# Optimization experiments

Hardware: AMD Instinct MI355X
Metric: run time of the kernel (lower is better)

Reference implementation:

```python
import jax, jax.numpy as jnp
import numpy as np

D_MODEL = 768
N_HEAD = 12


def setup_inputs() -> dict:
    key = jax.random.key(0)
    k1, k2, k3, k4, k5 = jax.random.split(key, 5)
    B, T, C = 4, 2048, D_MODEL
    s = 1.0 / np.sqrt(C)
    return {
        "x": jax.random.normal(k1, (B, T, C), dtype=jnp.float32),
        "w_attn": jax.random.normal(k2, (C, 3 * C), dtype=jnp.float32) * s,
        "b_attn": jax.random.normal(k3, (3 * C,), dtype=jnp.float32) * 0.02,
        "w_proj": jax.random.normal(k4, (C, C), dtype=jnp.float32) * s,
        "b_proj": jax.random.normal(k5, (C,), dtype=jnp.float32) * 0.02,
    }


def reference(x, w_attn, b_attn, w_proj, b_proj):
    B, T, C = x.shape
    H = N_HEAD
    Dh = C // H
    qkv = x @ w_attn + b_attn                      # [B, T, 3C]
    q, k, v = jnp.split(qkv, 3, axis=-1)
    # [B, H, T, Dh]
    q = q.reshape(B, T, H, Dh).transpose(0, 2, 1, 3)
    k = k.reshape(B, T, H, Dh).transpose(0, 2, 1, 3)
    v = v.reshape(B, T, H, Dh).transpose(0, 2, 1, 3)
    att = jnp.einsum("bhqd,bhkd->bhqk", q, k) * (1.0 / np.sqrt(Dh))
    causal = jnp.tril(jnp.ones((T, T), dtype=bool))
    att = jnp.where(causal[None, None, :, :], att, -jnp.inf)
    att = jax.nn.softmax(att, axis=-1)             # dropout p=0 (eval)
    y = jnp.einsum("bhqk,bhkd->bhqd", att, v)      # [B, H, T, Dh]
    y = y.transpose(0, 2, 1, 3).reshape(B, T, C)
    return y @ w_proj + b_proj
```

## Files before the change

kernel.cpp:

```cpp
#include <hip/hip_runtime.h>
#include <stdint.h>

#define NHEAD 12
#define DH 64
#define BATCH 4
#define SEQ 2048
#define CDIM 768
#define MROWS (BATCH*SEQ)

typedef __attribute__((ext_vector_type(8))) short short8;
typedef __attribute__((ext_vector_type(4))) float floatx4;
typedef unsigned int u32;

__device__ inline unsigned short f2bf(float f) {
    union { float f; unsigned u; } v; v.f = f;
    unsigned r = v.u + 0x7FFFu + ((v.u >> 16) & 1u);
    return (unsigned short)(r >> 16);
}

__device__ __forceinline__ u32 pk_bf16(float a, float b) {
    u32 d;
    asm("v_cvt_pk_bf16_f32 %0, %1, %2" : "=v"(d) : "v"(a), "v"(b));
    return d;
}

__device__ __forceinline__ void async_cp16(const unsigned short* g, unsigned short* l) {
    __builtin_amdgcn_global_load_lds(
        (const __attribute__((address_space(1))) u32*)g,
        (__attribute__((address_space(3))) u32*)l, 16, 0, 0);
}

__global__ void convert_f32_bf16(const float* __restrict__ in,
                                 unsigned short* __restrict__ out, int n) {
    int i = (blockIdx.x * blockDim.x + threadIdx.x) * 4;
    if (i + 3 < n) {
        float4 f = *(const float4*)(in + i);
        union { unsigned short s[4]; uint2 u; } p;
        p.s[0] = f2bf(f.x); p.s[1] = f2bf(f.y);
        p.s[2] = f2bf(f.z); p.s[3] = f2bf(f.w);
        *(uint2*)(out + i) = p.u;
    }
}

__global__ __launch_bounds__(256) void transpose_conv(
    const float* __restrict__ in, unsigned short* __restrict__ out,
    int K, int N) {
    __shared__ unsigned short T[64][72];
    const int k0 = blockIdx.x * 64, n0 = blockIdx.y * 64;
    const int t = threadIdx.x;
    const int nc = t & 63, kw = t >> 6;
    for (int i = 0; i < 16; i++) {
        const int kr = kw + i * 4;
        T[nc][kr] = f2bf(in[(size_t)(k0 + kr) * N + n0 + nc]);
    }
    __syncthreads();
    const int row = t >> 2, seg = t & 3;
    uint4 a = *(const uint4*)&T[row][seg * 16];
    uint4 b2 = *(const uint4*)&T[row][seg * 16 + 8];
    unsigned short* o = &out[(size_t)(n0 + row) * K + k0 + seg * 16];
    *(uint4*)o = a;
    *(uint4*)(o + 8) = b2;
}

template<int MODE>
__global__ __launch_bounds__(256) void gemm_bf16(
    const unsigned short* __restrict__ A,
    const unsigned short* __restrict__ BT,
    const float* __restrict__ bias,
    float* __restrict__ Cout,
    unsigned short* __restrict__ Qout,
    unsigned short* __restrict__ Kout,
    unsigned short* __restrict__ VTout,
    int Ndim, int Kdim)
{
    __shared__ unsigned short As[2][128 * 32];
    __shared__ unsigned short Bs[2][128 * 32];
    const int tid  = threadIdx.x;
    const int wave = tid >> 6;
    const int lane = tid & 63;
    const int l16  = lane & 15;
    const int quad = lane >> 4;
    const int wm = wave >> 1, wn = wave & 1;
    const int m0 = blockIdx.x * 128;
    const int n0 = blockIdx.y * 128;

    const int rloc = lane >> 2;
    const int gs   = ((lane & 3) ^ (rloc & 3) ^ ((rloc >> 2) & 3)) * 8;
    const int ar0  = wave * 32 + rloc;
    const int pg = ((quad ^ (l16 & 3) ^ ((l16 >> 2) & 3))) * 8;

    floatx4 acc[4][4];
    for (int i = 0; i < 4; i++)
        for (int j = 0; j < 4; j++) acc[i][j] = (floatx4)0.0f;

    for (int ch = 0; ch < 2; ch++) {
        const int row = ar0 + ch * 16;
        async_cp16(&A[(size_t)(m0 + row) * Kdim + gs], &As[0][(wave * 2 + ch) * 512]);
        async_cp16(&BT[(size_t)(n0 + row) * Kdim + gs], &Bs[0][(wave * 2 + ch) * 512]);
    }
    __syncthreads();

    for (int k0 = 0; k0 < Kdim; k0 += 32) {
        const int cur = (k0 >> 5) & 1;
        if (k0 + 32 < Kdim) {
            for (int ch = 0; ch < 2; ch++) {
                const int row = ar0 + ch * 16;
                async_cp16(&A[(size_t)(m0 + row) * Kdim + k0 + 32 + gs],
                           &As[cur ^ 1][(wave * 2 + ch) * 512]);
                async_cp16(&BT[(size_t)(n0 + row) * Kdim + k0 + 32 + gs],
                           &Bs[cur ^ 1][(wave * 2 + ch) * 512]);
            }
        }
        short8 a[4], b[4];
        for (int i = 0; i < 4; i++)
            a[i] = *(const short8*)&As[cur][(wm * 64 + i * 16 + l16) * 32 + pg];
        for (int j = 0; j < 4; j++)
            b[j] = *(const short8*)&Bs[cur][(wn * 64 + j * 16 + l16) * 32 + pg];
        for (int i = 0; i < 4; i++)
            for (int j = 0; j < 4; j++)
                acc[i][j] = __builtin_amdgcn_mfma_f32_16x16x32_bf16(
                    a[i], b[j], acc[i][j], 0, 0, 0);
        __syncthreads();
    }

    const float QSCALE = 0.18033688011112042f;
    for (int i = 0; i < 4; i++) {
        const int mbase = m0 + wm * 64 + i * 16 + quad * 4;
        for (int j = 0; j < 4; j++) {
            const int ncol = n0 + wn * 64 + j * 16 + l16;
            const float bv = bias[ncol];
            for (int r = 0; r < 4; r++) {
                const int m = mbase + r;
                const float v = acc[i][j][r] + bv;
                if (MODE == 0) {
                    Cout[(size_t)m * Ndim + ncol] = v;
                } else {
                    const int b_  = m >> 11, t = m & 2047;
                    const int part = ncol / CDIM;
                    const int c = ncol - part * CDIM;
                    const int h = c >> 6, d = c & 63;
                    const size_t bh = (size_t)(b_ * NHEAD + h);
                    if (part == 0)
                        Qout[(bh * SEQ + t) * DH + d] = f2bf(v * QSCALE);
                    else if (part == 1)
                        Kout[(bh * SEQ + t) * DH + d] = f2bf(v);
                    else
                        VTout[(bh * DH + d) * SEQ + t] = f2bf(v);
                }
            }
        }
    }
}

__global__ __launch_bounds__(256) void attn_kernel(
    const unsigned short* __restrict__ Q,
    const unsigned short* __restrict__ K,
    const unsigned short* __restrict__ VT,
    unsigned short* __restrict__ O)
{
    __shared__ unsigned short Kl[2][2][64 * 32];
    __shared__ unsigned short Vl[2][2][64 * 32];
    __shared__ unsigned short Pl[4][16 * 68];

    const int tid  = threadIdx.x;
    const int wave = tid >> 6;
    const int lane = tid & 63;
    const int l16  = lane & 15;
    const int quad = lane >> 4;

    const int lin = blockIdx.x;
    const int grp = lin >> 3;
    const int xs  = grp & 15;
    const int bh  = ((grp >> 4) << 3) | (lin & 7);
    const int h = bh % NHEAD, b = bh / NHEAD;

    const unsigned short* Qp = Q  + (size_t)bh * SEQ * DH;
    const unsigned short* Kp = K  + (size_t)bh * SEQ * DH;
    const unsigned short* Vp = VT + (size_t)bh * DH * SEQ;

    const int rloc = lane >> 2;
    const int gofsK = ((lane & 3) ^ (rloc & 3) ^ ((rloc >> 2) & 3)) * 8;
    const int pg = ((quad ^ (l16 & 3) ^ ((l16 >> 2) & 3))) * 8;

    for (int pass = 0; pass < 2; pass++) {
        const int qtile = pass == 0 ? xs : 31 - xs;
        const int qb = qtile * 64;
        const int qw = qb + wave * 16;
        const int nkt = qtile + 1;

        short8 aq[2];
        for (int c = 0; c < 2; c++)
            aq[c] = *(const short8*)&Qp[(size_t)(qw + l16) * DH + c * 32 + quad * 8];

        floatx4 accO[4];
        for (int dt = 0; dt < 4; dt++) accO[dt] = (floatx4)0.0f;
        float lp = 0.0f;

        {
            const int krow = wave * 16 + rloc;
            for (int c = 0; c < 2; c++) {
                async_cp16(&Kp[(size_t)krow * DH + c * 32 + gofsK],
                           &Kl[0][c][wave * 512]);
                async_cp16(&Vp[(size_t)krow * SEQ + 0 + c * 32 + gofsK],
                           &Vl[0][c][wave * 512]);
            }
        }
        __syncthreads();

        for (int kt = 0; kt < nkt; kt++) {
            const int kb  = kt * 64;
            const int cur = kt & 1;

            if (kt + 1 < nkt) {
                const int kbn = kb + 64;
                const int krow = wave * 16 + rloc;
                for (int c = 0; c < 2; c++) {
                    async_cp16(&Kp[(size_t)(kbn + krow) * DH + c * 32 + gofsK],
                               &Kl[cur ^ 1][c][wave * 512]);
                    async_cp16(&Vp[(size_t)krow * SEQ + kbn + c * 32 + gofsK],
                               &Vl[cur ^ 1][c][wave * 512]);
                }
            }

            floatx4 s[4];
            for (int jn = 0; jn < 4; jn++) {
                s[jn] = (floatx4)0.0f;
                for (int c = 0; c < 2; c++) {
                    short8 bk = *(const short8*)
                        &Kl[cur][c][(jn * 16 + l16) * 32 + pg];
                    s[jn] = __builtin_amdgcn_mfma_f32_16x16x32_bf16(
                        bk, aq[c], s[jn], 0, 0, 0);
                }
            }

            if (kt == nkt - 1) {
                const int q = qw + l16;
                for (int jn = 0; jn < 4; jn++) {
                    const int key = kb + jn * 16 + quad * 4;
                    for (int r = 0; r < 4; r++)
                        if (key + r > q) s[jn][r] = -1e30f;
                }
            }

            for (int jn = 0; jn < 4; jn++)
                for (int r = 0; r < 4; r++) {
                    float p = exp2f(s[jn][r]);
                    s[jn][r] = p;
                    lp += p;
                }

            for (int jn = 0; jn < 4; jn++) {
                uint2 u;
                u.x = pk_bf16(s[jn][0], s[jn][1]);
                u.y = pk_bf16(s[jn][2], s[jn][3]);
                *(uint2*)&Pl[wave][l16 * 68 + jn * 16 + quad * 4] = u;
            }
            short8 ap[2];
            for (int c = 0; c < 2; c++) {
                union { short8 v; uint2 u2[2]; } a_;
                const int base = l16 * 68 + c * 32 + quad * 8;
                a_.u2[0] = *(const uint2*)&Pl[wave][base];
                a_.u2[1] = *(const uint2*)&Pl[wave][base + 4];
                ap[c] = a_.v;
            }

            for (int dt = 0; dt < 4; dt++)
                for (int c = 0; c < 2; c++) {
                    short8 bv = *(const short8*)
                        &Vl[cur][c][(dt * 16 + l16) * 32 + pg];
                    accO[dt] = __builtin_amdgcn_mfma_f32_16x16x32_bf16(
                        ap[c], bv, accO[dt], 0, 0, 0);
                }

            __syncthreads();
        }

        float L = lp;
        L += __shfl_xor(L, 16);
        L += __shfl_xor(L, 32);
        for (int r = 0; r < 4; r++) {
            const float Lr = __shfl(L, (lane & 48) | (quad * 4 + r), 64);
            const float inv = 1.0f / Lr;
            const int t = qb + wave * 16 + quad * 4 + r;
            const size_t base = ((size_t)b * SEQ + t) * CDIM + h * DH;
            for (int dt = 0; dt < 4; dt++)
                O[base + dt * 16 + l16] = f2bf(accO[dt][r] * inv);
        }
        __syncthreads();
    }
}

extern "C" void kernel_launch(void* const* d_in, const int* in_sizes, int n_in,
                              void* d_out, int out_size, void* d_ws, size_t ws_size,
                              hipStream_t stream) {
    const float* x      = (const float*)d_in[0];
    const float* w_attn = (const float*)d_in[1];
    const float* b_attn = (const float*)d_in[2];
    const float* w_proj = (const float*)d_in[3];
    const float* b_proj = (const float*)d_in[4];
    float* out = (float*)d_out;

    unsigned short* xb   = (unsigned short*)d_ws;
    unsigned short* wta  = xb  + (size_t)MROWS * CDIM;
    unsigned short* wtp  = wta + (size_t)3 * CDIM * CDIM;
    unsigned short* qws  = wtp + (size_t)CDIM * CDIM;
    unsigned short* kws  = qws + (size_t)MROWS * CDIM;
    unsigned short* vtws = kws + (size_t)MROWS * CDIM;
    unsigned short* ob   = xb;

    const int nx = MROWS * CDIM;
    convert_f32_bf16<<<nx / 1024, 256, 0, stream>>>(x, xb, nx);
    transpose_conv<<<dim3(CDIM / 64, 3 * CDIM / 64), 256, 0, stream>>>(
        w_attn, wta, CDIM, 3 * CDIM);
    transpose_conv<<<dim3(CDIM / 64, CDIM / 64), 256, 0, stream>>>(
        w_proj, wtp, CDIM, CDIM);

    dim3 g1(MROWS / 128, (3 * CDIM) / 128);
    gemm_bf16<1><<<g1, 256, 0, stream>>>(xb, wta, b_attn, nullptr,
                                         qws, kws, vtws, 3 * CDIM, CDIM);

    attn_kernel<<<768, 256, 0, stream>>>(qws, kws, vtws, ob);

    dim3 g3(MROWS / 128, CDIM / 128);
    gemm_bf16<0><<<g3, 256, 0, stream>>>(ob, wtp, b_proj, out,
                                         nullptr, nullptr, nullptr, CDIM, CDIM);
}
```

Baseline: 223.2 us.

## Triple-buffer GEMM pipeline with vmcnt waits, smaller proj tiles, leaner attention sync

The GEMM moves from double to triple buffering. Tiles are staged two steps ahead, and explicit s_waitcnt vmcnt plus s_barrier replace the per-iteration __syncthreads, so loads overlap compute and barriers are fewer. The output-projection GEMM uses 64x64 tiles to launch more blocks for its small N. The attention loop merges its two barriers into one waitcnt+barrier at the top of each step. Manual vmcnt counts depend on the exact number of outstanding loads, so a miscount could cause races, and the smaller tiles lower data reuse.

New measurement: 226.2 us. About the same (+1.3%).

```diff
diff --git a/kernel.cpp b/kernel.cpp
--- a/kernel.cpp
+++ b/kernel.cpp
@@ -62,7 +62,7 @@
     *(uint4*)(o + 8) = b2;
 }
 
-template<int MODE>
+template<int MODE, int KD, int BMN>
 __global__ __launch_bounds__(256) void gemm_bf16(
     const unsigned short* __restrict__ A,
     const unsigned short* __restrict__ BT,
@@ -71,75 +71,91 @@
     unsigned short* __restrict__ Qout,
     unsigned short* __restrict__ Kout,
     unsigned short* __restrict__ VTout,
-    int Ndim, int Kdim)
+    int Ndim)
 {
-    __shared__ unsigned short As[2][128 * 32];
-    __shared__ unsigned short Bs[2][128 * 32];
+    constexpr int TMN = BMN / 32;
+    constexpr int CH  = BMN / 64;
+    __shared__ unsigned short As[3][BMN * 32];
+    __shared__ unsigned short Bs[3][BMN * 32];
     const int tid  = threadIdx.x;
     const int wave = tid >> 6;
     const int lane = tid & 63;
     const int l16  = lane & 15;
     const int quad = lane >> 4;
     const int wm = wave >> 1, wn = wave & 1;
-    const int m0 = blockIdx.x * 128;
-    const int n0 = blockIdx.y * 128;
+    const int m0 = blockIdx.x * BMN;
+    const int n0 = blockIdx.y * BMN;
 
     const int rloc = lane >> 2;
-    const int gs   = ((lane & 3) ^ (rloc & 3) ^ ((rloc >> 2) & 3)) * 8;
-    const int ar0  = wave * 32 + rloc;
-    const int pg = ((quad ^ (l16 & 3) ^ ((l16 >> 2) & 3))) * 8;
-
-    floatx4 acc[4][4];
-    for (int i = 0; i < 4; i++)
-        for (int j = 0; j < 4; j++) acc[i][j] = (floatx4)0.0f;
-
-    for (int ch = 0; ch < 2; ch++) {
-        const int row = ar0 + ch * 16;
-        async_cp16(&A[(size_t)(m0 + row) * Kdim + gs], &As[0][(wave * 2 + ch) * 512]);
-        async_cp16(&BT[(size_t)(n0 + row) * Kdim + gs], &Bs[0][(wave * 2 + ch) * 512]);
-    }
-    __syncthreads();
-
-    for (int k0 = 0; k0 < Kdim; k0 += 32) {
-        const int cur = (k0 >> 5) & 1;
-        if (k0 + 32 < Kdim) {
-            for (int ch = 0; ch < 2; ch++) {
-                const int row = ar0 + ch * 16;
-                async_cp16(&A[(size_t)(m0 + row) * Kdim + k0 + 32 + gs],
-                           &As[cur ^ 1][(wave * 2 + ch) * 512]);
-                async_cp16(&BT[(size_t)(n0 + row) * Kdim + k0 + 32 + gs],
-                           &Bs[cur ^ 1][(wave * 2 + ch) * 512]);
-            }
-        }
-        short8 a[4], b[4];
-        for (int i = 0; i < 4; i++)
-            a[i] = *(const short8*)&As[cur][(wm * 64 + i * 16 + l16) * 32 + pg];
-        for (int j = 0; j < 4; j++)
-            b[j] = *(const short8*)&Bs[cur][(wn * 64 + j * 16 + l16) * 32 + pg];
-        for (int i = 0; i < 4; i++)
-            for (int j = 0; j < 4; j++)
+    const int gs   = (((lane & 3) ^ (rloc & 3) ^ ((rloc >> 2) & 3))) * 8;
+    const int ar0  = wave * (BMN / 4) + rloc;
+    const int pg   = ((quad ^ (l16 & 3) ^ ((l16 >> 2) & 3))) * 8;
+
+    floatx4 acc[TMN][TMN];
+    for (int i = 0; i < TMN; i++)
+        for (int j = 0; j < TMN; j++) acc[i][j] = (floatx4)0.0f;
+
+    constexpr int NIT = KD / 32;
+
+    auto stageTo = [&](int s, int buf) {
+        const int koff = s * 32;
+        for (int ch = 0; ch < CH; ch++) {
+            const int row = ar0 + ch * 16;
+            async_cp16(&A[(size_t)(m0 + row) * KD + koff + gs],
+                       &As[buf][(wave * CH + ch) * 512]);
+            async_cp16(&BT[(size_t)(n0 + row) * KD + koff + gs],
+                       &Bs[buf][(wave * CH + ch) * 512]);
+        }
+    };
+    stageTo(0, 0);
+    stageTo(1, 1);
+
+    int buf = 0;
+    for (int it = 0; it < NIT; it++) {
+        if (it < NIT - 1) {
+            if constexpr (BMN == 128)
+                asm volatile("s_waitcnt vmcnt(4)" ::: "memory");
+            else
+                asm volatile("s_waitcnt vmcnt(2)" ::: "memory");
+        } else {
+            asm volatile("s_waitcnt vmcnt(0)" ::: "memory");
+        }
+        asm volatile("s_barrier" ::: "memory");
+        if (it + 2 < NIT) {
+            int b2 = buf + 2; if (b2 >= 3) b2 -= 3;
+            stageTo(it + 2, b2);
+        }
+        short8 a[TMN], b[TMN];
+        for (int i = 0; i < TMN; i++)
+            a[i] = *(const short8*)&As[buf][(wm * (BMN / 2) + i * 16 + l16) * 32 + pg];
+        for (int j = 0; j < TMN; j++)
+            b[j] = *(const short8*)&Bs[buf][(wn * (BMN / 2) + j * 16 + l16) * 32 + pg];
+        for (int i = 0; i < TMN; i++)
+            for (int j = 0; j < TMN; j++)
                 acc[i][j] = __builtin_amdgcn_mfma_f32_16x16x32_bf16(
                     a[i], b[j], acc[i][j], 0, 0, 0);
-        __syncthreads();
+        buf++; if (buf >= 3) buf = 0;
     }
 
     const float QSCALE = 0.18033688011112042f;
-    for (int i = 0; i < 4; i++) {
-        const int mbase = m0 + wm * 64 + i * 16 + quad * 4;
-        for (int j = 0; j < 4; j++) {
-            const int ncol = n0 + wn * 64 + j * 16 + l16;
+    for (int i = 0; i < TMN; i++) {
+        const int mbase = m0 + wm * (BMN / 2) + i * 16 + quad * 4;
+        for (int j = 0; j < TMN; j++) {
+            const int ncj  = n0 + wn * (BMN / 2) + j * 16;
+            const int part = ncj / CDIM;
+            const int cj   = ncj - part * CDIM;
+            const int ncol = ncj + l16;
             const float bv = bias[ncol];
+            const int c = cj + l16;
+            const int hh = c >> 6, d = c & 63;
             for (int r = 0; r < 4; r++) {
                 const int m = mbase + r;
                 const float v = acc[i][j][r] + bv;
                 if (MODE == 0) {
                     Cout[(size_t)m * Ndim + ncol] = v;
                 } else {
-                    const int b_  = m >> 11, t = m & 2047;
-                    const int part = ncol / CDIM;
-                    const int c = ncol - part * CDIM;
-                    const int h = c >> 6, d = c & 63;
-                    const size_t bh = (size_t)(b_ * NHEAD + h);
+                    const int b_ = m >> 11, t = m & 2047;
+                    const size_t bh = (size_t)(b_ * NHEAD + hh);
                     if (part == 0)
                         Qout[(bh * SEQ + t) * DH + d] = f2bf(v * QSCALE);
                     else if (part == 1)
@@ -181,6 +197,7 @@
     const int rloc = lane >> 2;
     const int gofsK = ((lane & 3) ^ (rloc & 3) ^ ((rloc >> 2) & 3)) * 8;
     const int pg = ((quad ^ (l16 & 3) ^ ((l16 >> 2) & 3))) * 8;
+    const int krow = wave * 16 + rloc;
 
     for (int pass = 0; pass < 2; pass++) {
         const int qtile = pass == 0 ? xs : 31 - xs;
@@ -196,24 +213,22 @@
         for (int dt = 0; dt < 4; dt++) accO[dt] = (floatx4)0.0f;
         float lp = 0.0f;
 
-        {
-            const int krow = wave * 16 + rloc;
-            for (int c = 0; c < 2; c++) {
-                async_cp16(&Kp[(size_t)krow * DH + c * 32 + gofsK],
-                           &Kl[0][c][wave * 512]);
-                async_cp16(&Vp[(size_t)krow * SEQ + 0 + c * 32 + gofsK],
-                           &Vl[0][c][wave * 512]);
-            }
-        }
-        __syncthreads();
+        for (int c = 0; c < 2; c++) {
+            async_cp16(&Kp[(size_t)krow * DH + c * 32 + gofsK],
+                       &Kl[0][c][wave * 512]);
+            async_cp16(&Vp[(size_t)krow * SEQ + 0 + c * 32 + gofsK],
+                       &Vl[0][c][wave * 512]);
+        }
 
         for (int kt = 0; kt < nkt; kt++) {
             const int kb  = kt * 64;
             const int cur = kt & 1;
 
+            asm volatile("s_waitcnt vmcnt(0)" ::: "memory");
+            asm volatile("s_barrier" ::: "memory");
+
             if (kt + 1 < nkt) {
                 const int kbn = kb + 64;
-                const int krow = wave * 16 + rloc;
                 for (int c = 0; c < 2; c++) {
                     async_cp16(&Kp[(size_t)(kbn + krow) * DH + c * 32 + gofsK],
                                &Kl[cur ^ 1][c][wave * 512]);
@@ -271,8 +286,6 @@
                     accO[dt] = __builtin_amdgcn_mfma_f32_16x16x32_bf16(
                         ap[c], bv, accO[dt], 0, 0, 0);
                 }
-
-            __syncthreads();
         }
 
         float L = lp;
@@ -316,12 +329,12 @@
         w_proj, wtp, CDIM, CDIM);
 
     dim3 g1(MROWS / 128, (3 * CDIM) / 128);
-    gemm_bf16<1><<<g1, 256, 0, stream>>>(xb, wta, b_attn, nullptr,
-                                         qws, kws, vtws, 3 * CDIM, CDIM);
+    gemm_bf16<1, CDIM, 128><<<g1, 256, 0, stream>>>(xb, wta, b_attn, nullptr,
+                                                    qws, kws, vtws, 3 * CDIM);
 
     attn_kernel<<<768, 256, 0, stream>>>(qws, kws, vtws, ob);
 
-    dim3 g3(MROWS / 128, CDIM / 128);
-    gemm_bf16<0><<<g3, 256, 0, stream>>>(ob, wtp, b_proj, out,
-                                         nullptr, nullptr, nullptr, CDIM, CDIM);
-}
+    dim3 g3(MROWS / 64, CDIM / 64);
+    gemm_bf16<0, CDIM, 64><<<g3, 256, 0, stream>>>(ob, wtp, b_proj, out,
+                                                   nullptr, nullptr, nullptr, CDIM);
+}
```
